# Performance work log

Hardware: AMD Instinct MI355X
Metric: run time of the kernel (lower is better)

The kernel has to match this reference:

```python
import jax, jax.numpy as jnp
import numpy as np

C = 1.0          # curvature parameter (constraint <x,x>_L = -1/C)
EPS = 1e-7
N_NODES = 50000
D = 128
N_EDGES = 800000


def _l_inner(u, v):
    # Lorentz (Minkowski) inner product: -u0*v0 + <u_s, v_s>
    return -u[..., 0] * v[..., 0] + jnp.sum(u[..., 1:] * v[..., 1:], axis=-1)


def _proj(x, c=C):
    # recompute time coordinate so x lies on the hyperboloid
    sp = x[:, 1:]
    x0 = jnp.sqrt(1.0 / c + jnp.sum(sp * sp, axis=-1, keepdims=True))
    return jnp.concatenate([x0, sp], axis=-1)


def _logmap0(x, c=C):
    sqc = jnp.sqrt(c)
    x0, sp = x[:, :1], x[:, 1:]
    y = jnp.clip(sqc * x0, 1.0 + EPS, None)
    d = jnp.arccosh(y) / sqc                                   # geodesic distance to origin
    sn = jnp.clip(jnp.linalg.norm(sp, axis=-1, keepdims=True), EPS, None)
    return jnp.concatenate([jnp.zeros_like(x0), d * sp / sn], axis=-1)


def _expmap0(u, c=C):
    sqc = jnp.sqrt(c)
    sp = u[:, 1:]
    un = jnp.clip(jnp.linalg.norm(sp, axis=-1, keepdims=True), EPS, None)
    th = sqc * un
    x0 = jnp.cosh(th) / sqc
    return jnp.concatenate([x0, jnp.sinh(th) * sp / th], axis=-1)


def setup_inputs() -> dict:
    key = jax.random.key(0)
    k1, k2, k3 = jax.random.split(key, 3)
    x_raw = jax.random.normal(k1, (N_NODES, D), dtype=jnp.float32) * 0.5
    x = _proj(x_raw)  # valid points on the Lorentz manifold
    # xavier-uniform-like scale for (127,127) weight
    lim = float(np.sqrt(6.0 / (2 * (D - 1))))
    weight = jax.random.uniform(k2, (D - 1, D - 1), dtype=jnp.float32, minval=-lim, maxval=lim)
    bias = jnp.zeros((D - 1,), dtype=jnp.float32)
    edge_index = jax.random.randint(k3, (2, N_EDGES), 0, N_NODES, dtype=jnp.int64)
    return {"x": x, "weight": weight, "bias": bias, "edge_index": edge_index}


def reference(x, weight, bias, edge_index):
    c = C
    # ---- HyperbolicLinear (lorentz): log0 -> spatial matmul + bias -> exp0 -> proj
    v = _logmap0(x, c)                         # [N, D], time comp = 0
    out_space = v[:, 1:] @ weight.T + bias     # [N, D-1]
    out = jnp.concatenate([v[:, :1], out_space], axis=-1)
    h = _proj(_expmap0(out, c), c)             # [N, D] on manifold
    # ---- HyperbolicDistAtt: gather -> lorentz distance -> exp(-d)
    row, col = edge_index[0], edge_index[1]
    xi = h[row]                                # [E, D]
    xj = h[col]                                # [E, D]
    inner = _l_inner(xi, xj)                   # [E]
    dist = jnp.arccosh(jnp.clip(-c * inner, 1.0 + EPS, None)) / jnp.sqrt(c)
    att = jnp.exp(-dist)                       # [E]
    # ---- Lorentz centroid: weighted sum then Minkowski-norm normalization
    num = jax.ops.segment_sum(att[:, None] * xj, row, num_segments=h.shape[0])  # [N, D]
    denom = jnp.sqrt(c) * jnp.sqrt(jnp.clip(-_l_inner(num, num), EPS, None))    # [N]
    return num / denom[:, None]
```

## Files before the change

### kernel.cpp

```cpp
#include <hip/hip_runtime.h>
#include <math.h>

#define EPS 1e-7f
#define CAP 64
#define REC_INTS   34
#define REC_USH    68
#define LIST_OFF    4

typedef __attribute__((ext_vector_type(8))) short short8;
typedef __attribute__((ext_vector_type(4))) float floatx4;

__device__ inline short f2bf(float f) {
    union { float f; unsigned u; } v; v.f = f;
    unsigned r = v.u + 0x7FFF + ((v.u >> 16) & 1);
    return (short)(r >> 16);
}

__device__ inline float fast_sqrt(float x) { return __builtin_amdgcn_sqrtf(x); }
__device__ inline float fast_rcp(float x)  { return __builtin_amdgcn_rcpf(x); }
__device__ inline float fast_rsq(float x)  { return __builtin_amdgcn_rsqf(x); }

__global__ __launch_bounds__(256) void prep_w(
    const float* __restrict__ weight, short* __restrict__ wfg,
    int* __restrict__ rec, int N)
{
    int idx = blockIdx.x * 256 + threadIdx.x;
    if (idx < 128 * 128) {
        int j = idx >> 7, k = idx & 127;
        float w = (j < 127 && k >= 1) ? weight[j * 127 + (k - 1)] : 0.0f;
        int tt = j >> 4, cc = j & 15, ss = k >> 5, qq = (k >> 3) & 3, ee = k & 7;
        wfg[(((tt * 4 + ss) * 64) + qq * 16 + cc) * 8 + ee] = f2bf(w);
    }
    if (rec) {
        for (int r = idx; r < N; r += gridDim.x * 256) rec[(size_t)r * REC_INTS] = 0;
    }
}

__global__ __launch_bounds__(256) void transform_mfma(
    const float* __restrict__ x, const short* __restrict__ wfg,
    const float* __restrict__ bias, float* __restrict__ h, int N)
{
    __shared__ __align__(16) short Wf[8 * 4 * 64 * 8];
    __shared__ __align__(16) short Vf[4 * 4 * 64 * 8];

    const int t = threadIdx.x;
    const int lane = t & 63;
    const int wv = t >> 6;
    const int c = lane & 15;
    const int q = lane >> 4;

    {
        const short8* src = (const short8*)wfg;
        short8* dst = (short8*)Wf;
        #pragma unroll
        for (int it = 0; it < 8; ++it) dst[it * 256 + t] = src[it * 256 + t];
    }
    float bvals[8];
    #pragma unroll
    for (int tt = 0; tt < 8; ++tt) {
        int j = tt * 16 + c;
        bvals[tt] = (j < 127) ? bias[j] : 0.0f;
    }
    __syncthreads();

    const short8* wfp = (const short8*)Wf;
    const short8* vfp = (const short8*)Vf + wv * 256;
    short8* vw = (short8*)Vf;

    const int nchunks = (N + 63) >> 6;
    for (int chunk = blockIdx.x; chunk < nchunks; chunk += gridDim.x) {
        const int base = chunk * 64;

        {
            int nl = t >> 2;
            int qt = t & 3;
            int n = base + nl;
            const float4* xr = (const float4*)(x + (size_t)n * 128 + qt * 32);
            float4 xv[8];
            if (n < N) {
                #pragma unroll
                for (int g = 0; g < 8; ++g) xv[g] = xr[g];
            } else {
                #pragma unroll
                for (int g = 0; g < 8; ++g) xv[g] = make_float4(0, 0, 0, 0);
            }
            float ss = 0.0f;
            #pragma unroll
            for (int g = 0; g < 8; ++g)
                ss += xv[g].x * xv[g].x + xv[g].y * xv[g].y +
                      xv[g].z * xv[g].z + xv[g].w * xv[g].w;
            float x0 = xv[0].x;
            if (qt == 0) ss -= x0 * x0;
            ss += __shfl_xor(ss, 1, 64);
            ss += __shfl_xor(ss, 2, 64);
            x0 = __shfl(x0, lane & ~3, 64);
            float sn = fmaxf(fast_sqrt(ss), EPS);
            float xc = fmaxf(x0, 1.0f + EPS);
            float dd = __logf(xc + fast_sqrt(xc * xc - 1.0f));
            float coef = dd * fast_rcp(sn);
            int wreg = nl >> 4, cn = nl & 15;
            #pragma unroll
            for (int g = 0; g < 4; ++g) {
                float4 a = xv[2 * g], b = xv[2 * g + 1];
                short8 pk;
                pk[0] = f2bf(coef * a.x); pk[1] = f2bf(coef * a.y);
                pk[2] = f2bf(coef * a.z); pk[3] = f2bf(coef * a.w);
                pk[4] = f2bf(coef * b.x); pk[5] = f2bf(coef * b.y);
                pk[6] = f2bf(coef * b.z); pk[7] = f2bf(coef * b.w);
                vw[wreg * 256 + qt * 64 + g * 16 + cn] = pk;
            }
        }

        floatx4 acc[8];
        #pragma unroll
        for (int tt = 0; tt < 8; ++tt) acc[tt] = (floatx4){0, 0, 0, 0};
        #pragma unroll
        for (int s = 0; s < 4; ++s) {
            short8 af = vfp[s * 64 + lane];
            #pragma unroll
            for (int tt = 0; tt < 8; ++tt) {
                short8 bf = wfp[(tt * 4 + s) * 64 + lane];
                acc[tt] = __builtin_amdgcn_mfma_f32_16x16x32_bf16(af, bf, acc[tt], 0, 0, 0);
            }
        }

        float rs[4] = {0, 0, 0, 0};
        #pragma unroll
        for (int tt = 0; tt < 8; ++tt) {
            #pragma unroll
            for (int r = 0; r < 4; ++r) {
                float v = acc[tt][r] + bvals[tt];
                acc[tt][r] = v;
                rs[r] += v * v;
            }
        }
        #pragma unroll
        for (int r = 0; r < 4; ++r) {
            rs[r] += __shfl_xor(rs[r], 1, 64);
            rs[r] += __shfl_xor(rs[r], 2, 64);
            rs[r] += __shfl_xor(rs[r], 4, 64);
            rs[r] += __shfl_xor(rs[r], 8, 64);
        }
        int nodebase = base + wv * 16 + q * 4;
        #pragma unroll
        for (int r = 0; r < 4; ++r) {
            int n = nodebase + r;
            if (n < N) {
                float th = fmaxf(fast_sqrt(rs[r]), EPS);
                float ex = __expf(th);
                float sc_big = (ex - fast_rcp(ex)) * 0.5f * fast_rcp(th);
                float sc_small = 1.0f + th * th * (1.0f / 6.0f);
                float scale = (th < 1e-3f) ? sc_small : sc_big;
                float* hr = h + (size_t)n * 128;
                #pragma unroll
                for (int tt = 0; tt < 8; ++tt) {
                    int j = tt * 16 + c;
                    if (j < 127) hr[1 + j] = scale * acc[tt][r];
                    else         hr[0] = fast_sqrt(1.0f + scale * scale * rs[r]);
                }
            }
        }
    }
}

__global__ __launch_bounds__(256) void scatter_cap(
    const int* __restrict__ rows, const int* __restrict__ cols,
    int* __restrict__ rec, int E)
{
    int i = blockIdx.x * 256 + threadIdx.x;
    if (i < E) {
        int r = rows[i];
        int p = atomicAdd(rec + (size_t)r * REC_INTS, 1);
        if (p < CAP)
            ((ushort*)rec)[(size_t)r * REC_USH + LIST_OFF + p] = (ushort)cols[i];
    }
}

__global__ __launch_bounds__(256) void agg_cap(
    const float* __restrict__ h, const int* __restrict__ rec,
    float* __restrict__ out, int N)
{
    int wid = (int)((blockIdx.x * 256u + threadIdx.x) >> 6);
    int nw = (int)(gridDim.x * 4u);
    int lane = threadIdx.x & 63;
    int q = lane >> 4;
    int i = lane & 15;

    for (int n = wid; n < N; n += nw) {
        int deg = rec[(size_t)n * REC_INTS];
        if (deg > CAP) deg = CAP;
        const ushort* lst = (const ushort*)rec + (size_t)n * REC_USH + LIST_OFF;
        int ec = (lane < deg) ? (int)lst[lane] : 0;

        const float4* hn = (const float4*)(h + (size_t)n * 128) + 2 * i;
        float4 xa = hn[0], xb = hn[1];
        float xa0 = (i == 0) ? -xa.x : xa.x;
        float acc[8] = {0, 0, 0, 0, 0, 0, 0, 0};

        for (int kb = 0; kb < deg; kb += 16) {
            int k0 = kb + q;
            bool v0 = k0      < deg;
            bool v1 = k0 + 4  < deg;
            bool v2 = k0 + 8  < deg;
            bool v3 = k0 + 12 < deg;
            int c0 = __shfl(ec, k0,      64);
            int c1 = __shfl(ec, k0 + 4,  64);
            int c2 = __shfl(ec, k0 + 8,  64);
            int c3 = __shfl(ec, k0 + 12, 64);
            float4 a0 = {0,0,0,0}, b0 = {0,0,0,0};
            float4 a1 = {0,0,0,0}, b1 = {0,0,0,0};
            float4 a2 = {0,0,0,0}, b2 = {0,0,0,0};
            float4 a3 = {0,0,0,0}, b3 = {0,0,0,0};
            if (v0) { const float4* p = (const float4*)(h + (size_t)c0 * 128) + 2 * i; a0 = p[0]; b0 = p[1]; }
            if (v1) { const float4* p = (const float4*)(h + (size_t)c1 * 128) + 2 * i; a1 = p[0]; b1 = p[1]; }
            if (v2) { const float4* p = (const float4*)(h + (size_t)c2 * 128) + 2 * i; a2 = p[0]; b2 = p[1]; }
            if (v3) { const float4* p = (const float4*)(h + (size_t)c3 * 128) + 2 * i; a3 = p[0]; b3 = p[1]; }

            float s0 = xa0 * a0.x + xa.y * a0.y + xa.z * a0.z + xa.w * a0.w
                     + xb.x * b0.x + xb.y * b0.y + xb.z * b0.z + xb.w * b0.w;
            float s1 = xa0 * a1.x + xa.y * a1.y + xa.z * a1.z + xa.w * a1.w
                     + xb.x * b1.x + xb.y * b1.y + xb.z * b1.z + xb.w * b1.w;
            float s2 = xa0 * a2.x + xa.y * a2.y + xa.z * a2.z + xa.w * a2.w
                     + xb.x * b2.x + xb.y * b2.y + xb.z * b2.z + xb.w * b2.w;
            float s3 = xa0 * a3.x + xa.y * a3.y + xa.z * a3.z + xa.w * a3.w
                     + xb.x * b3.x + xb.y * b3.y + xb.z * b3.z + xb.w * b3.w;
            #pragma unroll
            for (int o = 1; o <= 8; o <<= 1) {
                s0 += __shfl_xor(s0, o, 64);
                s1 += __shfl_xor(s1, o, 64);
                s2 += __shfl_xor(s2, o, 64);
                s3 += __shfl_xor(s3, o, 64);
            }
            float z0 = fmaxf(-s0, 1.0f + EPS);
            float z1 = fmaxf(-s1, 1.0f + EPS);
            float z2 = fmaxf(-s2, 1.0f + EPS);
            float z3 = fmaxf(-s3, 1.0f + EPS);
            float att0 = v0 ? fast_rcp(z0 + fast_sqrt(z0 * z0 - 1.0f)) : 0.0f;
            float att1 = v1 ? fast_rcp(z1 + fast_sqrt(z1 * z1 - 1.0f)) : 0.0f;
            float att2 = v2 ? fast_rcp(z2 + fast_sqrt(z2 * z2 - 1.0f)) : 0.0f;
            float att3 = v3 ? fast_rcp(z3 + fast_sqrt(z3 * z3 - 1.0f)) : 0.0f;
            acc[0] += att0 * a0.x + att1 * a1.x + att2 * a2.x + att3 * a3.x;
            acc[1] += att0 * a0.y + att1 * a1.y + att2 * a2.y + att3 * a3.y;
            acc[2] += att0 * a0.z + att1 * a1.z + att2 * a2.z + att3 * a3.z;
            acc[3] += att0 * a0.w + att1 * a1.w + att2 * a2.w + att3 * a3.w;
            acc[4] += att0 * b0.x + att1 * b1.x + att2 * b2.x + att3 * b3.x;
            acc[5] += att0 * b0.y + att1 * b1.y + att2 * b2.y + att3 * b3.y;
            acc[6] += att0 * b0.z + att1 * b1.z + att2 * b2.z + att3 * b3.z;
            acc[7] += att0 * b0.w + att1 * b1.w + att2 * b2.w + att3 * b3.w;
        }

        #pragma unroll
        for (int k = 0; k < 8; ++k) {
            acc[k] += __shfl_xor(acc[k], 16, 64);
            acc[k] += __shfl_xor(acc[k], 32, 64);
        }

        float part = 0.0f;
        #pragma unroll
        for (int k = 0; k < 8; ++k) part -= acc[k] * acc[k];
        if (i == 0) part += 2.0f * acc[0] * acc[0];
        #pragma unroll
        for (int o = 1; o <= 8; o <<= 1) part += __shfl_xor(part, o, 64);
        float inv = fast_rsq(fmaxf(part, EPS));

        if (q == 0) {
            float4* op = (float4*)(out + (size_t)n * 128) + 2 * i;
            op[0] = make_float4(acc[0] * inv, acc[1] * inv, acc[2] * inv, acc[3] * inv);
            op[1] = make_float4(acc[4] * inv, acc[5] * inv, acc[6] * inv, acc[7] * inv);
        }
    }
}

__global__ __launch_bounds__(256) void hist_kernel(
    const int* __restrict__ rows, int* __restrict__ deg, int E)
{
    int i = blockIdx.x * 256 + threadIdx.x;
    if (i < E) atomicAdd(&deg[rows[i]], 1);
}

__global__ __launch_bounds__(1024) void scan1(
    const int* __restrict__ deg, int* __restrict__ off,
    int* __restrict__ bsum, int N)
{
    __shared__ int wsum[16];
    __shared__ int wexcl[16];
    int i = blockIdx.x * 1024 + threadIdx.x;
    int lane = threadIdx.x & 63, wid = threadIdx.x >> 6;
    int v = (i < N) ? deg[i] : 0;
    int incl = v;
    #pragma unroll
    for (int o = 1; o < 64; o <<= 1) {
        int u = __shfl_up(incl, o, 64);
        if (lane >= o) incl += u;
    }
    if (lane == 63) wsum[wid] = incl;
    __syncthreads();
    if (wid == 0 && lane < 16) {
        int s = wsum[lane];
        int si = s;
        #pragma unroll
        for (int o = 1; o < 16; o <<= 1) {
            int u = __shfl_up(si, o, 64);
            if (lane >= o) si += u;
        }
        wexcl[lane] = si - s;
        if (lane == 15) bsum[blockIdx.x] = si;
    }
    __syncthreads();
    if (i < N) off[i] = wexcl[wid] + incl - v;
}

__global__ __launch_bounds__(64) void scan2(int* __restrict__ bsum, int nb)
{
    int lane = threadIdx.x & 63;
    int v = (lane < nb) ? bsum[lane] : 0;
    int si = v;
    #pragma unroll
    for (int o = 1; o < 64; o <<= 1) {
        int u = __shfl_up(si, o, 64);
        if (lane >= o) si += u;
    }
    if (lane < nb) bsum[lane] = si - v;
}

__global__ __launch_bounds__(1024) void scan3(
    int* __restrict__ off, int* __restrict__ pos,
    const int* __restrict__ bsum, int N, int E)
{
    int i = blockIdx.x * 1024 + threadIdx.x;
    if (i < N) {
        int v = off[i] + bsum[blockIdx.x];
        off[i] = v;
        pos[i] = v;
    }
    if (i == 0) off[N] = E;
}

__global__ __launch_bounds__(256) void scatter_kernel(
    const int* __restrict__ rows, const int* __restrict__ cols,
    int* __restrict__ pos, int* __restrict__ ecol, int E)
{
    int i = blockIdx.x * 256 + threadIdx.x;
    if (i < E) {
        int p = atomicAdd(&pos[rows[i]], 1);
        ecol[p] = cols[i];
    }
}

__global__ __launch_bounds__(256) void agg_kernel(
    const float* __restrict__ h, const int* __restrict__ off,
    const int* __restrict__ ecol, float* __restrict__ out, int N)
{
    int wid = (int)((blockIdx.x * 256u + threadIdx.x) >> 6);
    int nw = (int)(gridDim.x * 4u);
    int lane = threadIdx.x & 63;
    int q = lane >> 4;
    int i = lane & 15;

    for (int n = wid; n < N; n += nw) {
        const float4* hn = (const float4*)(h + (size_t)n * 128) + 2 * i;
        float4 xa = hn[0], xb = hn[1];
        float xa0 = (i == 0) ? -xa.x : xa.x;
        float acc[8] = {0, 0, 0, 0, 0, 0, 0, 0};
        int e0 = off[n], e1 = off[n + 1];

        int e = e0 + q;
        for (; e + 4 < e1; e += 8) {
            int c0 = ecol[e];
            int c1 = ecol[e + 4];
            const float4* p0 = (const float4*)(h + (size_t)c0 * 128) + 2 * i;
            const float4* p1 = (const float4*)(h + (size_t)c1 * 128) + 2 * i;
            float4 a0 = p0[0], b0 = p0[1];
            float4 a1 = p1[0], b1 = p1[1];
            float s0 = xa0 * a0.x + xa.y * a0.y + xa.z * a0.z + xa.w * a0.w
                     + xb.x * b0.x + xb.y * b0.y + xb.z * b0.z + xb.w * b0.w;
            float s1 = xa0 * a1.x + xa.y * a1.y + xa.z * a1.z + xa.w * a1.w
                     + xb.x * b1.x + xb.y * b1.y + xb.z * b1.z + xb.w * b1.w;
            #pragma unroll
            for (int o = 1; o <= 8; o <<= 1) {
                s0 += __shfl_xor(s0, o, 64);
                s1 += __shfl_xor(s1, o, 64);
            }
            float z0 = fmaxf(-s0, 1.0f + EPS);
            float z1 = fmaxf(-s1, 1.0f + EPS);
            float att0 = fast_rcp(z0 + fast_sqrt(z0 * z0 - 1.0f));
            float att1 = fast_rcp(z1 + fast_sqrt(z1 * z1 - 1.0f));
            acc[0] += att0 * a0.x + att1 * a1.x;
            acc[1] += att0 * a0.y + att1 * a1.y;
            acc[2] += att0 * a0.z + att1 * a1.z;
            acc[3] += att0 * a0.w + att1 * a1.w;
            acc[4] += att0 * b0.x + att1 * b1.x;
            acc[5] += att0 * b0.y + att1 * b1.y;
            acc[6] += att0 * b0.z + att1 * b1.z;
            acc[7] += att0 * b0.w + att1 * b1.w;
        }
        if (e < e1) {
            int c0 = ecol[e];
            const float4* p0 = (const float4*)(h + (size_t)c0 * 128) + 2 * i;
            float4 a0 = p0[0], b0 = p0[1];
            float s0 = xa0 * a0.x + xa.y * a0.y + xa.z * a0.z + xa.w * a0.w
                     + xb.x * b0.x + xb.y * b0.y + xb.z * b0.z + xb.w * b0.w;
            #pragma unroll
            for (int o = 1; o <= 8; o <<= 1) s0 += __shfl_xor(s0, o, 64);
            float z0 = fmaxf(-s0, 1.0f + EPS);
            float att0 = fast_rcp(z0 + fast_sqrt(z0 * z0 - 1.0f));
            acc[0] += att0 * a0.x;
            acc[1] += att0 * a0.y;
            acc[2] += att0 * a0.z;
            acc[3] += att0 * a0.w;
            acc[4] += att0 * b0.x;
            acc[5] += att0 * b0.y;
            acc[6] += att0 * b0.z;
            acc[7] += att0 * b0.w;
        }

        #pragma unroll
        for (int k = 0; k < 8; ++k) {
            acc[k] += __shfl_xor(acc[k], 16, 64);
            acc[k] += __shfl_xor(acc[k], 32, 64);
        }

        float part = 0.0f;
        #pragma unroll
        for (int k = 0; k < 8; ++k) part -= acc[k] * acc[k];
        if (i == 0) part += 2.0f * acc[0] * acc[0];
        #pragma unroll
        for (int o = 1; o <= 8; o <<= 1) part += __shfl_xor(part, o, 64);
        float inv = fast_rsq(fmaxf(part, EPS));

        if (q == 0) {
            float4* op = (float4*)(out + (size_t)n * 128) + 2 * i;
            op[0] = make_float4(acc[0] * inv, acc[1] * inv, acc[2] * inv, acc[3] * inv);
            op[1] = make_float4(acc[4] * inv, acc[5] * inv, acc[6] * inv, acc[7] * inv);
        }
    }
}

__global__ __launch_bounds__(256) void edge_kernel(
    const float* __restrict__ h, const int* __restrict__ rows,
    const int* __restrict__ cols, float* __restrict__ num, int E)
{
    int wid = (int)((blockIdx.x * 256u + threadIdx.x) >> 6);
    if (wid >= E) return;
    int lane = threadIdx.x & 63;
    int r = rows[wid];
    int c = cols[wid];
    const float2* h2 = (const float2*)h;
    float2 xi = h2[(size_t)r * 64 + lane];
    float2 xj = h2[(size_t)c * 64 + lane];
    float p = (lane == 0 ? -xi.x * xj.x : xi.x * xj.x) + xi.y * xj.y;
    #pragma unroll
    for (int off = 32; off >= 1; off >>= 1) p += __shfl_xor(p, off, 64);
    float z = fmaxf(-p, 1.0f + EPS);
    float att = fast_rcp(z + fast_sqrt(z * z - 1.0f));
    float* dst = num + (size_t)r * 128 + 2 * lane;
    atomicAdd(dst, att * xj.x);
    atomicAdd(dst + 1, att * xj.y);
}

__global__ __launch_bounds__(256) void norm_kernel(float* __restrict__ num, int N)
{
    int wid = (int)((blockIdx.x * 256u + threadIdx.x) >> 6);
    int nw = (int)((gridDim.x * 256u) >> 6);
    int lane = threadIdx.x & 63;
    for (int n = wid; n < N; n += nw) {
        float2* p2 = (float2*)(num + (size_t)n * 128);
        float2 v = p2[lane];
        float q = (lane == 0) ? (v.x * v.x - v.y * v.y) : (-v.x * v.x - v.y * v.y);
        #pragma unroll
        for (int o = 32; o >= 1; o >>= 1) q += __shfl_xor(q, o, 64);
        float inv = fast_rsq(fmaxf(q, EPS));
        p2[lane] = make_float2(v.x * inv, v.y * inv);
    }
}

extern "C" void kernel_launch(void* const* d_in, const int* in_sizes, int n_in,
                              void* d_out, int out_size, void* d_ws, size_t ws_size,
                              hipStream_t stream)
{
    const float* x      = (const float*)d_in[0];
    const float* weight = (const float*)d_in[1];
    const float* bias   = (const float*)d_in[2];
    const int*   edge   = (const int*)d_in[3];

    const int N = in_sizes[0] / 128;
    const int E = in_sizes[3] / 2;
    const int* rows = edge;
    const int* cols = edge + E;

    char* base = (char*)d_ws;
    float* h   = (float*)base;                       base += (size_t)N * 128 * 4;
    short* wfg = (short*)base;                       base += (size_t)128 * 128 * 2;
    char* rest = base;
    size_t head = (size_t)(rest - (char*)d_ws);

    int* rec = (int*)rest;
    size_t need_cap = head + (size_t)N * REC_INTS * 4;

    int* deg  = (int*)rest;
    int* off  = deg + N;
    int* pos  = off + (N + 1);
    int* bsum = pos + N;
    int* ecol = bsum + 64;
    size_t need_csr = head + ((size_t)N * 3 + 65 + E) * 4;

    const int nchunks = (N + 63) >> 6;

    if (ws_size >= need_cap && N <= 65535) {
        prep_w<<<64, 256, 0, stream>>>(weight, wfg, rec, N);
        transform_mfma<<<nchunks, 256, 0, stream>>>(x, wfg, bias, h, N);
        scatter_cap<<<(E + 255) / 256, 256, 0, stream>>>(rows, cols, rec, E);
        agg_cap<<<(N + 3) / 4, 256, 0, stream>>>(h, rec, (float*)d_out, N);
    } else if (ws_size >= need_csr) {
        prep_w<<<64, 256, 0, stream>>>(weight, wfg, deg, N);
        transform_mfma<<<nchunks, 256, 0, stream>>>(x, wfg, bias, h, N);
        const int nsb = (N + 1023) / 1024;
        hist_kernel<<<(E + 255) / 256, 256, 0, stream>>>(rows, deg, E);
        scan1<<<nsb, 1024, 0, stream>>>(deg, off, bsum, N);
        scan2<<<1, 64, 0, stream>>>(bsum, nsb);
        scan3<<<nsb, 1024, 0, stream>>>(off, pos, bsum, N, E);
        scatter_kernel<<<(E + 255) / 256, 256, 0, stream>>>(rows, cols, pos, ecol, E);
        agg_kernel<<<(N + 3) / 4, 256, 0, stream>>>(h, off, ecol, (float*)d_out, N);
    } else {
        prep_w<<<64, 256, 0, stream>>>(weight, wfg, (int*)nullptr, 0);
        transform_mfma<<<nchunks, 256, 0, stream>>>(x, wfg, bias, h, N);
        hipMemsetAsync(d_out, 0, (size_t)out_size * sizeof(float), stream);
        edge_kernel<<<(E + 3) / 4, 256, 0, stream>>>(h, rows, cols, (float*)d_out, E);
        norm_kernel<<<2048, 256, 0, stream>>>((float*)d_out, N);
    }
}
```

Before: 189.2 us.

## Fuse node transform and edge scatter into one interleaved kernel launch

Merges the MFMA node transform and the capped-list edge scatter into a single launch. Transform blocks are interleaved among scatter blocks so both kinds of work run concurrently on the GPU instead of back to back. Edge index loads become nontemporal, and the prep kernel grid grows to speed up record zeroing. The interleaving adds block-index arithmetic and mixes shared-memory-heavy blocks with atomic-heavy blocks, which may change occupancy.

```diff
diff --git a/kernel.cpp b/kernel.cpp
--- a/kernel.cpp
+++ b/kernel.cpp
@@ -36,9 +36,10 @@
     }
 }
 
-__global__ __launch_bounds__(256) void transform_mfma(
+__device__ __forceinline__ void transform_body(
     const float* __restrict__ x, const short* __restrict__ wfg,
-    const float* __restrict__ bias, float* __restrict__ h, int N)
+    const float* __restrict__ bias, float* __restrict__ h, int N,
+    int chunk0, int cstride)
 {
     __shared__ __align__(16) short Wf[8 * 4 * 64 * 8];
     __shared__ __align__(16) short Vf[4 * 4 * 64 * 8];
@@ -68,7 +69,7 @@
     short8* vw = (short8*)Vf;
 
     const int nchunks = (N + 63) >> 6;
-    for (int chunk = blockIdx.x; chunk < nchunks; chunk += gridDim.x) {
+    for (int chunk = chunk0; chunk < nchunks; chunk += cstride) {
         const int base = chunk * 64;
 
         {
@@ -163,16 +164,48 @@
     }
 }
 
+__global__ __launch_bounds__(256) void transform_mfma(
+    const float* __restrict__ x, const short* __restrict__ wfg,
+    const float* __restrict__ bias, float* __restrict__ h, int N)
+{
+    transform_body(x, wfg, bias, h, N, blockIdx.x, gridDim.x);
+}
+
+__device__ __forceinline__ void scatter_edge(
+    const int* __restrict__ rows, const int* __restrict__ cols,
+    int* __restrict__ rec, int E, int i)
+{
+    if (i < E) {
+        int r  = __builtin_nontemporal_load(rows + i);
+        int cc = __builtin_nontemporal_load(cols + i);
+        int p = atomicAdd(rec + (size_t)r * REC_INTS, 1);
+        if (p < CAP)
+            ((ushort*)rec)[(size_t)r * REC_USH + LIST_OFF + p] = (ushort)cc;
+    }
+}
+
 __global__ __launch_bounds__(256) void scatter_cap(
     const int* __restrict__ rows, const int* __restrict__ cols,
     int* __restrict__ rec, int E)
 {
-    int i = blockIdx.x * 256 + threadIdx.x;
-    if (i < E) {
-        int r = rows[i];
-        int p = atomicAdd(rec + (size_t)r * REC_INTS, 1);
-        if (p < CAP)
-            ((ushort*)rec)[(size_t)r * REC_USH + LIST_OFF + p] = (ushort)cols[i];
+    scatter_edge(rows, cols, rec, E, blockIdx.x * 256 + threadIdx.x);
+}
+
+__global__ __launch_bounds__(256) void fused_ts(
+    const float* __restrict__ x, const short* __restrict__ wfg,
+    const float* __restrict__ bias, float* __restrict__ h, int N,
+    const int* __restrict__ rows, const int* __restrict__ cols,
+    int* __restrict__ rec, int E, int T, int K)
+{
+    int bid = (int)blockIdx.x;
+    int m = bid / K;
+    int r = bid - m * K;
+    if (r == 0 && m < T) {
+        transform_body(x, wfg, bias, h, N, m, (int)gridDim.x);
+    } else {
+        int before = (r == 0) ? T : (m + 1 < T ? m + 1 : T);
+        int sb = bid - before;
+        scatter_edge(rows, cols, rec, E, sb * 256 + (int)threadIdx.x);
     }
 }
 
@@ -507,12 +540,14 @@
     const int nchunks = (N + 63) >> 6;
 
     if (ws_size >= need_cap && N <= 65535) {
-        prep_w<<<64, 256, 0, stream>>>(weight, wfg, rec, N);
-        transform_mfma<<<nchunks, 256, 0, stream>>>(x, wfg, bias, h, N);
-        scatter_cap<<<(E + 255) / 256, 256, 0, stream>>>(rows, cols, rec, E);
+        const int T = nchunks;
+        const int S = (E + 255) / 256;
+        const int K = (T + S) / T > 0 ? (T + S) / T : 1;
+        prep_w<<<256, 256, 0, stream>>>(weight, wfg, rec, N);
+        fused_ts<<<T + S, 256, 0, stream>>>(x, wfg, bias, h, N, rows, cols, rec, E, T, K);
         agg_cap<<<(N + 3) / 4, 256, 0, stream>>>(h, rec, (float*)d_out, N);
     } else if (ws_size >= need_csr) {
-        prep_w<<<64, 256, 0, stream>>>(weight, wfg, deg, N);
+        prep_w<<<256, 256, 0, stream>>>(weight, wfg, deg, N);
         transform_mfma<<<nchunks, 256, 0, stream>>>(x, wfg, bias, h, N);
         const int nsb = (N + 1023) / 1024;
         hist_kernel<<<(E + 255) / 256, 256, 0, stream>>>(rows, deg, E);
@@ -522,7 +557,7 @@
         scatter_kernel<<<(E + 255) / 256, 256, 0, stream>>>(rows, cols, pos, ecol, E);
         agg_kernel<<<(N + 3) / 4, 256, 0, stream>>>(h, off, ecol, (float*)d_out, N);
     } else {
-        prep_w<<<64, 256, 0, stream>>>(weight, wfg, (int*)nullptr, 0);
+        prep_w<<<256, 256, 0, stream>>>(weight, wfg, (int*)nullptr, 0);
         transform_mfma<<<nchunks, 256, 0, stream>>>(x, wfg, bias, h, N);
         hipMemsetAsync(d_out, 0, (size_t)out_size * sizeof(float), stream);
         edge_kernel<<<(E + 3) / 4, 256, 0, stream>>>(h, rows, cols, (float*)d_out, E);
```

After: 196.3 us. 3.8% more time.
